# Kernel optimization log

Measured on AMD Instinct MI355X. Metric: run time of the kernel, lower is better.

The kernel has to match this reference:

```python
import jax, jax.numpy as jnp
import numpy as np

DIM = 768
HEADS = 12
HEAD_DIM = DIM // HEADS
SCALE = HEAD_DIM ** -0.5


def setup_inputs() -> dict:
    key = jax.random.key(0)
    k_x, k_qkv, k_ow, k_ob = jax.random.split(key, 4)
    B, N = 8, 1024
    x = jax.random.normal(k_x, (B, N, DIM), dtype=jnp.float32)
    # nn.Linear weights: out = x @ W.T + b; store torch-layout [out, in]
    w_qkv = jax.random.normal(k_qkv, (3 * DIM, DIM), dtype=jnp.float32) * (DIM ** -0.5)
    w_out = jax.random.normal(k_ow, (DIM, DIM), dtype=jnp.float32) * (DIM ** -0.5)
    b_out = jax.random.normal(k_ob, (DIM,), dtype=jnp.float32) * 0.01
    return {"x": x, "w_qkv": w_qkv, "w_out": w_out, "b_out": b_out}


def reference(x, w_qkv, w_out, b_out):
    B, N, C = x.shape
    qkv = jnp.einsum('bnc,dc->bnd', x, w_qkv)            # [B, N, 3C]
    qkv = qkv.reshape(B, N, 3, HEADS, HEAD_DIM)
    qkv = jnp.transpose(qkv, (2, 0, 3, 1, 4))            # [3, B, H, N, Dh]
    q, k, v = qkv[0], qkv[1], qkv[2]
    attn = jnp.einsum('bhqd,bhkd->bhqk', q, k) * SCALE   # [B, H, N, N]
    attn = jax.nn.softmax(attn, axis=-1)
    o = jnp.einsum('bhqk,bhkd->bhqd', attn, v)           # [B, H, N, Dh]
    o = jnp.transpose(o, (0, 2, 1, 3)).reshape(B, N, C)
    return jnp.einsum('bnc,dc->bnd', o, w_out) + b_out
```

## Files before the change

kernel.cpp:

```cpp
#include <hip/hip_runtime.h>

#define B_ 8
#define N_ 1024
#define DIM_ 768
#define H_ 12
#define DH_ 64
#define M_ (B_ * N_)
#define NQKV_ (3 * DIM_)
#define SCL_ 0.18033688011112042f

typedef unsigned short u16;
typedef unsigned int u32;
typedef __attribute__((ext_vector_type(8))) unsigned short u16x8;
typedef __attribute__((ext_vector_type(4))) unsigned short u16x4;
typedef __attribute__((ext_vector_type(8))) short bf16x8;
typedef __attribute__((ext_vector_type(4))) float f32x4;

__device__ __forceinline__ u16 f2bf(float f) {
  u32 u = __builtin_bit_cast(u32, f);
  u += 0x7fffu + ((u >> 16) & 1u);
  return (u16)(u >> 16);
}
__device__ __forceinline__ float bf2f(u16 v) {
  u32 u = ((u32)v) << 16;
  return __builtin_bit_cast(float, u);
}
__device__ __forceinline__ u32 cvtpk_bf16(float lo, float hi) {
  u32 r;
  asm("v_cvt_pk_bf16_f32 %0, %1, %2" : "=v"(r) : "v"(lo), "v"(hi));
  return r;
}
__device__ __forceinline__ void async16(const void* g, void* l) {
  __builtin_amdgcn_global_load_lds(
      (const __attribute__((address_space(1))) unsigned int*)g,
      (__attribute__((address_space(3))) unsigned int*)l, 16, 0, 0);
}

__global__ __launch_bounds__(256) void cast_bf16_k(const float* __restrict__ in,
                                                   u16* __restrict__ out, int n4) {
  int i = blockIdx.x * 256 + threadIdx.x;
  if (i >= n4) return;
  float4 v = reinterpret_cast<const float4*>(in)[i];
  u16x4 o;
  o.x = f2bf(v.x); o.y = f2bf(v.y); o.z = f2bf(v.z); o.w = f2bf(v.w);
  reinterpret_cast<u16x4*>(out)[i] = o;
}

template <bool OUT_BF16, bool BIAS, bool VSPLIT>
__global__ __launch_bounds__(256) void gemm_bt_k(
    const u16* __restrict__ A, const u16* __restrict__ Bm,
    void* __restrict__ Cv, const float* __restrict__ bias, int K, int ldc,
    u16* __restrict__ vT) {
  __shared__ u16 As[128 * 32];
  __shared__ u16 Bs[128 * 32];
  const int t = threadIdx.x;
  const int lane = t & 63;
  const int wid = t >> 6;
  const int brow = blockIdx.y << 7;
  const int bcol = blockIdx.x << 7;
  const int wrow = (wid >> 1) << 6;
  const int wcol = (wid & 1) << 6;

  f32x4 acc[4][4];
#pragma unroll
  for (int m = 0; m < 4; ++m)
#pragma unroll
    for (int n = 0; n < 4; ++n) acc[m][n] = (f32x4){0.f, 0.f, 0.f, 0.f};

  const int loff0 = t << 4, loff1 = (t + 256) << 4;
  const int r0 = loff0 >> 6, r1 = loff1 >> 6;
  const int s0 = ((((loff0 >> 4) & 3) ^ (r0 & 3)) << 3);
  const int s1 = ((((loff1 >> 4) & 3) ^ (r1 & 3)) << 3);
  const u16* gA0 = A + (size_t)(brow + r0) * K + s0;
  const u16* gA1 = A + (size_t)(brow + r1) * K + s1;
  const u16* gB0 = Bm + (size_t)(bcol + r0) * K + s0;
  const u16* gB1 = Bm + (size_t)(bcol + r1) * K + s1;
  char* lA = (char*)As;
  char* lB = (char*)Bs;

  const int kb = (lane >> 4) << 4;
  int aoff[4], boff[4];
#pragma unroll
  for (int m = 0; m < 4; ++m) {
    int ra = wrow + (m << 4) + (lane & 15);
    aoff[m] = (ra << 6) + (kb ^ ((ra & 3) << 4));
    int rb = wcol + (m << 4) + (lane & 15);
    boff[m] = (rb << 6) + (kb ^ ((rb & 3) << 4));
  }

  const int nkt = K >> 5;
  for (int kt = 0; kt < nkt; ++kt) {
    const int ko = kt << 5;
    async16(gA0 + ko, lA + loff0);
    async16(gA1 + ko, lA + loff1);
    async16(gB0 + ko, lB + loff0);
    async16(gB1 + ko, lB + loff1);
    __syncthreads();
    bf16x8 af[4], bfr[4];
#pragma unroll
    for (int m = 0; m < 4; ++m) af[m] = *(const bf16x8*)(lA + aoff[m]);
#pragma unroll
    for (int n = 0; n < 4; ++n) bfr[n] = *(const bf16x8*)(lB + boff[n]);
#pragma unroll
    for (int m = 0; m < 4; ++m)
#pragma unroll
      for (int n = 0; n < 4; ++n)
        acc[m][n] = __builtin_amdgcn_mfma_f32_16x16x32_bf16(af[m], bfr[n],
                                                            acc[m][n], 0, 0, 0);
    __syncthreads();
  }

  const int crow = brow + wrow + ((lane >> 4) << 2);
  const int ccol0 = bcol + wcol + (lane & 15);
  if (VSPLIT && bcol >= 2 * DIM_) {
#pragma unroll
    for (int n = 0; n < 4; ++n) {
      int colh = ccol0 + (n << 4) - 2 * DIM_;
      int h = colh >> 6, d = colh & 63;
#pragma unroll
      for (int m = 0; m < 4; ++m) {
        int row0 = crow + (m << 4);
        int bb = row0 >> 10, nn = row0 & 1023;
        int hbl = bb * H_ + h;
        uint2 pk;
        pk.x = (u32)f2bf(acc[m][n][0]) | ((u32)f2bf(acc[m][n][1]) << 16);
        pk.y = (u32)f2bf(acc[m][n][2]) | ((u32)f2bf(acc[m][n][3]) << 16);
        *(uint2*)(vT + (((size_t)(hbl * 64 + d)) << 10) + nn) = pk;
      }
    }
    return;
  }
#pragma unroll
  for (int m = 0; m < 4; ++m)
#pragma unroll
    for (int n = 0; n < 4; ++n) {
      int col = ccol0 + (n << 4);
      float bv = BIAS ? bias[col] : 0.f;
#pragma unroll
      for (int j = 0; j < 4; ++j) {
        int row = crow + (m << 4) + j;
        if (OUT_BF16)
          ((u16*)Cv)[(size_t)row * ldc + col] = f2bf(acc[m][n][j]);
        else
          ((float*)Cv)[(size_t)row * ldc + col] = acc[m][n][j] + bv;
      }
    }
}

__global__ __launch_bounds__(256) void attn_k(const u16* __restrict__ qkv,
                                              const u16* __restrict__ vT,
                                              u16* __restrict__ ob) {
  __shared__ u16 Ks[2][64 * 64];
  __shared__ u16 Vt[2][64 * 64];
  __shared__ u16 Ps[4][16 * 64];
  const int t = threadIdx.x;
  const int lane = t & 63;
  const int w = t >> 6;
  const int g = lane >> 4;
  const int q15 = lane & 15;

  const int orig = blockIdx.x;
  const int sub = orig >> 3;
  const int hb = (orig & 7) * 12 + (sub >> 4);
  const int qt = sub & 15;
  const int b = hb / H_;
  const int h = hb - b * H_;
  const int rowbase = b * N_;
  const int qcol = h * DH_;
  const int kcol = DIM_ + qcol;

  bf16x8 qf[2];
  {
    const int qrow = rowbase + (qt << 6) + (w << 4) + q15;
    const u16* src = qkv + (size_t)qrow * NQKV_ + qcol + (g << 3);
#pragma unroll
    for (int ks = 0; ks < 2; ++ks) {
      u16x8 raw = *(const u16x8*)(src + ks * 32);
      bf16x8 o;
#pragma unroll
      for (int j = 0; j < 8; ++j) o[j] = (short)f2bf(bf2f(raw[j]) * SCL_);
      qf[ks] = o;
    }
  }

  float mrow = -1e30f, lrow = 0.f;
  f32x4 oacc[4];
#pragma unroll
  for (int d = 0; d < 4; ++d) oacc[d] = (f32x4){0.f, 0.f, 0.f, 0.f};

  const int sr = t >> 3;
  const int c8 = t & 7;
  const int loff0 = t << 4, loff1 = (t + 256) << 4;
  const u16* kg0 = qkv + (size_t)(rowbase + sr) * NQKV_ + kcol + ((c8 ^ (sr & 7)) << 3);
  const u16* kg1 = qkv + (size_t)(rowbase + sr + 32) * NQKV_ + kcol + ((c8 ^ (sr & 7)) << 3);
  const u16* vg0 = vT + (((size_t)(hb * 64 + sr)) << 10) + ((c8 ^ (sr & 7)) << 3);
  const u16* vg1 = vT + (((size_t)(hb * 64 + sr + 32)) << 10) + ((c8 ^ (sr & 7)) << 3);
  char* lk0 = (char*)Ks;
  char* lv0 = (char*)Vt;
  char* lp = (char*)Ps + (w << 11);

  const int rowB = q15 << 7;
  const int xsw = (q15 & 7) << 4;
  const int x0 = (g << 4) ^ xsw;
  const int x1 = (64 + (g << 4)) ^ xsw;

  async16(kg0, lk0 + loff0);
  async16(kg1, lk0 + loff1);
  async16(vg0, lv0 + loff0);
  async16(vg1, lv0 + loff1);
  asm volatile("s_waitcnt vmcnt(0)" ::: "memory");
  __builtin_amdgcn_s_barrier();

  for (int kv = 0; kv < 16; ++kv) {
    const int cur = kv & 1;
    if (kv < 15) {
      const int nb = (cur ^ 1) << 13;
      const size_t kofs = (size_t)(kv + 1) * 64;
      async16(kg0 + kofs * NQKV_, lk0 + nb + loff0);
      async16(kg1 + kofs * NQKV_, lk0 + nb + loff1);
      async16(vg0 + kofs, lv0 + nb + loff0);
      async16(vg1 + kofs, lv0 + nb + loff1);
    }
    const char* lkc = lk0 + (cur << 13);
    const char* lvc = lv0 + (cur << 13);

    f32x4 s4[4];
#pragma unroll
    for (int n = 0; n < 4; ++n) s4[n] = (f32x4){0.f, 0.f, 0.f, 0.f};
    __builtin_amdgcn_s_setprio(1);
#pragma unroll
    for (int n = 0; n < 4; ++n) {
      bf16x8 kf0 = *(const bf16x8*)(lkc + (n << 11) + rowB + x0);
      s4[n] = __builtin_amdgcn_mfma_f32_16x16x32_bf16(kf0, qf[0], s4[n], 0, 0, 0);
      bf16x8 kf1 = *(const bf16x8*)(lkc + (n << 11) + rowB + x1);
      s4[n] = __builtin_amdgcn_mfma_f32_16x16x32_bf16(kf1, qf[1], s4[n], 0, 0, 0);
    }
    __builtin_amdgcn_s_setprio(0);

    float mx;
    {
      float a0 = fmaxf(fmaxf(s4[0][0], s4[0][1]), fmaxf(s4[0][2], s4[0][3]));
      float a1 = fmaxf(fmaxf(s4[1][0], s4[1][1]), fmaxf(s4[1][2], s4[1][3]));
      float a2 = fmaxf(fmaxf(s4[2][0], s4[2][1]), fmaxf(s4[2][2], s4[2][3]));
      float a3 = fmaxf(fmaxf(s4[3][0], s4[3][1]), fmaxf(s4[3][2], s4[3][3]));
      mx = fmaxf(fmaxf(a0, a1), fmaxf(a2, a3));
      mx = fmaxf(mx, __shfl_xor(mx, 16, 64));
      mx = fmaxf(mx, __shfl_xor(mx, 32, 64));
    }
    if (!__all(mx - mrow <= 8.f)) {
      float mn = fmaxf(mrow, mx);
      float al = __builtin_amdgcn_exp2f(mrow - mn);
      mrow = mn;
      lrow *= al;
      float alj[4];
#pragma unroll
      for (int j = 0; j < 4; ++j) alj[j] = __shfl(al, (g << 2) + j, 64);
#pragma unroll
      for (int d = 0; d < 4; ++d)
#pragma unroll
        for (int j = 0; j < 4; ++j) oacc[d][j] *= alj[j];
    }

    float p[4][4];
    float ps = 0.f;
#pragma unroll
    for (int n = 0; n < 4; ++n)
#pragma unroll
      for (int j = 0; j < 4; ++j) {
        p[n][j] = __builtin_amdgcn_exp2f(s4[n][j] - mrow);
        ps += p[n][j];
      }
    ps += __shfl_xor(ps, 16, 64);
    ps += __shfl_xor(ps, 32, 64);
    lrow += ps;

#pragma unroll
    for (int n = 0; n < 4; ++n) {
      uint2 pk;
      pk.x = cvtpk_bf16(p[n][0], p[n][1]);
      pk.y = cvtpk_bf16(p[n][2], p[n][3]);
      *(uint2*)(lp + rowB + (((n << 5) + (g << 3)) ^ xsw)) = pk;
    }

    bf16x8 pf0 = *(const bf16x8*)(lp + rowB + x0);
    bf16x8 pf1 = *(const bf16x8*)(lp + rowB + x1);
    __builtin_amdgcn_s_setprio(1);
#pragma unroll
    for (int dt = 0; dt < 4; ++dt) {
      bf16x8 vf0 = *(const bf16x8*)(lvc + (dt << 11) + rowB + x0);
      oacc[dt] = __builtin_amdgcn_mfma_f32_16x16x32_bf16(pf0, vf0, oacc[dt], 0, 0, 0);
      bf16x8 vf1 = *(const bf16x8*)(lvc + (dt << 11) + rowB + x1);
      oacc[dt] = __builtin_amdgcn_mfma_f32_16x16x32_bf16(pf1, vf1, oacc[dt], 0, 0, 0);
    }
    __builtin_amdgcn_s_setprio(0);

    asm volatile("s_waitcnt vmcnt(0)" ::: "memory");
    __builtin_amdgcn_s_barrier();
    __builtin_amdgcn_sched_barrier(0);
  }

  float rl = 1.f / lrow;
  float rlj[4];
#pragma unroll
  for (int j = 0; j < 4; ++j) rlj[j] = __shfl(rl, (g << 2) + j, 64);
  const int orow0 = rowbase + (qt << 6) + (w << 4) + (g << 2);
#pragma unroll
  for (int dt = 0; dt < 4; ++dt) {
    int col = qcol + (dt << 4) + q15;
#pragma unroll
    for (int j = 0; j < 4; ++j)
      ob[(size_t)(orow0 + j) * DIM_ + col] = f2bf(oacc[dt][j] * rlj[j]);
  }
}

extern "C" void kernel_launch(void* const* d_in, const int* in_sizes, int n_in,
                              void* d_out, int out_size, void* d_ws, size_t ws_size,
                              hipStream_t stream) {
  const float* x = (const float*)d_in[0];
  const float* w_qkv = (const float*)d_in[1];
  const float* w_out = (const float*)d_in[2];
  const float* b_out = (const float*)d_in[3];

  u16* xb = (u16*)d_ws;
  u16* wqkvb = xb + (size_t)M_ * DIM_;
  u16* woutb = wqkvb + (size_t)NQKV_ * DIM_;
  u16* qkvb = woutb + (size_t)DIM_ * DIM_;
  u16* obuf = qkvb + (size_t)M_ * NQKV_;
  u16* vT = obuf + (size_t)M_ * DIM_;

  {
    int n4 = M_ * DIM_ / 4;
    cast_bf16_k<<<(n4 + 255) / 256, 256, 0, stream>>>(x, xb, n4);
  }
  {
    int n4 = NQKV_ * DIM_ / 4;
    cast_bf16_k<<<(n4 + 255) / 256, 256, 0, stream>>>(w_qkv, wqkvb, n4);
  }
  {
    int n4 = DIM_ * DIM_ / 4;
    cast_bf16_k<<<(n4 + 255) / 256, 256, 0, stream>>>(w_out, woutb, n4);
  }

  gemm_bt_k<true, false, true><<<dim3(NQKV_ / 128, M_ / 128), 256, 0, stream>>>(
      xb, wqkvb, (void*)qkvb, nullptr, DIM_, NQKV_, vT);

  attn_k<<<dim3(B_ * H_ * 16), 256, 0, stream>>>(qkvb, vT, obuf);

  gemm_bt_k<false, true, false><<<dim3(DIM_ / 128, M_ / 128), 256, 0, stream>>>(
      obuf, woutb, d_out, b_out, DIM_, DIM_, nullptr);
}
```

Measured before the change: 213.2 us.

## Double-buffer GEMM LDS tiles and unroll attention loop by two

The QKV and output-projection GEMM kernel moves from a single LDS buffer, where each k-step loads and then waits, to a double-buffered ping-pong scheme. The next tile's async global-to-LDS load is issued before computing on the current one, with one vmcnt wait and barrier per step. The attention loop, which was already double-buffered, is unrolled by two with compile-time buffer offsets and incrementing pointers, removing runtime buffer selection. This doubles GEMM LDS use to 32KB per block, which could reduce occupancy.

```diff
diff --git a/kernel.cpp b/kernel.cpp
--- a/kernel.cpp
+++ b/kernel.cpp
@@ -35,6 +35,10 @@
       (const __attribute__((address_space(1))) unsigned int*)g,
       (__attribute__((address_space(3))) unsigned int*)l, 16, 0, 0);
 }
+#define VMCNT0_BARRIER()                                \
+  asm volatile("s_waitcnt vmcnt(0)" ::: "memory");      \
+  __builtin_amdgcn_s_barrier();                         \
+  __builtin_amdgcn_sched_barrier(0)
 
 __global__ __launch_bounds__(256) void cast_bf16_k(const float* __restrict__ in,
                                                    u16* __restrict__ out, int n4) {
@@ -46,13 +50,31 @@
   reinterpret_cast<u16x4*>(out)[i] = o;
 }
 
+template <int BUFO>
+__device__ __forceinline__ void gemm_step(const char* lA, const char* lB,
+                                          const int (&aoff)[4],
+                                          const int (&boff)[4],
+                                          f32x4 (&acc)[4][4]) {
+  bf16x8 af[4], bfr[4];
+#pragma unroll
+  for (int m = 0; m < 4; ++m) af[m] = *(const bf16x8*)(lA + BUFO + aoff[m]);
+#pragma unroll
+  for (int n = 0; n < 4; ++n) bfr[n] = *(const bf16x8*)(lB + BUFO + boff[n]);
+#pragma unroll
+  for (int m = 0; m < 4; ++m)
+#pragma unroll
+    for (int n = 0; n < 4; ++n)
+      acc[m][n] = __builtin_amdgcn_mfma_f32_16x16x32_bf16(af[m], bfr[n],
+                                                          acc[m][n], 0, 0, 0);
+}
+
 template <bool OUT_BF16, bool BIAS, bool VSPLIT>
 __global__ __launch_bounds__(256) void gemm_bt_k(
     const u16* __restrict__ A, const u16* __restrict__ Bm,
     void* __restrict__ Cv, const float* __restrict__ bias, int K, int ldc,
     u16* __restrict__ vT) {
-  __shared__ u16 As[128 * 32];
-  __shared__ u16 Bs[128 * 32];
+  __shared__ u16 As[2][128 * 32];
+  __shared__ u16 Bs[2][128 * 32];
   const int t = threadIdx.x;
   const int lane = t & 63;
   const int wid = t >> 6;
@@ -71,12 +93,21 @@
   const int r0 = loff0 >> 6, r1 = loff1 >> 6;
   const int s0 = ((((loff0 >> 4) & 3) ^ (r0 & 3)) << 3);
   const int s1 = ((((loff1 >> 4) & 3) ^ (r1 & 3)) << 3);
-  const u16* gA0 = A + (size_t)(brow + r0) * K + s0;
-  const u16* gA1 = A + (size_t)(brow + r1) * K + s1;
-  const u16* gB0 = Bm + (size_t)(bcol + r0) * K + s0;
-  const u16* gB1 = Bm + (size_t)(bcol + r1) * K + s1;
+  const u16* pA0 = A + (size_t)(brow + r0) * K + s0;
+  const u16* pA1 = A + (size_t)(brow + r1) * K + s1;
+  const u16* pB0 = Bm + (size_t)(bcol + r0) * K + s0;
+  const u16* pB1 = Bm + (size_t)(bcol + r1) * K + s1;
   char* lA = (char*)As;
   char* lB = (char*)Bs;
+
+#define GSTAGE(BUFO)                              \
+  do {                                            \
+    async16(pA0, lA + (BUFO) + loff0);            \
+    async16(pA1, lA + (BUFO) + loff1);            \
+    async16(pB0, lB + (BUFO) + loff0);            \
+    async16(pB1, lB + (BUFO) + loff1);            \
+    pA0 += 32; pA1 += 32; pB0 += 32; pB1 += 32;   \
+  } while (0)
 
   const int kb = (lane >> 4) << 4;
   int aoff[4], boff[4];
@@ -89,26 +120,17 @@
   }
 
   const int nkt = K >> 5;
-  for (int kt = 0; kt < nkt; ++kt) {
-    const int ko = kt << 5;
-    async16(gA0 + ko, lA + loff0);
-    async16(gA1 + ko, lA + loff1);
-    async16(gB0 + ko, lB + loff0);
-    async16(gB1 + ko, lB + loff1);
-    __syncthreads();
-    bf16x8 af[4], bfr[4];
-#pragma unroll
-    for (int m = 0; m < 4; ++m) af[m] = *(const bf16x8*)(lA + aoff[m]);
-#pragma unroll
-    for (int n = 0; n < 4; ++n) bfr[n] = *(const bf16x8*)(lB + boff[n]);
-#pragma unroll
-    for (int m = 0; m < 4; ++m)
-#pragma unroll
-      for (int n = 0; n < 4; ++n)
-        acc[m][n] = __builtin_amdgcn_mfma_f32_16x16x32_bf16(af[m], bfr[n],
-                                                            acc[m][n], 0, 0, 0);
-    __syncthreads();
-  }
+  GSTAGE(0);
+  VMCNT0_BARRIER();
+  for (int kt = 0; kt < nkt; kt += 2) {
+    GSTAGE(8192);
+    gemm_step<0>(lA, lB, aoff, boff, acc);
+    VMCNT0_BARRIER();
+    if (kt + 2 < nkt) GSTAGE(0);
+    gemm_step<8192>(lA, lB, aoff, boff, acc);
+    VMCNT0_BARRIER();
+  }
+#undef GSTAGE
 
   const int crow = brow + wrow + ((lane >> 4) << 2);
   const int ccol0 = bcol + wcol + (lane & 15);
@@ -147,6 +169,84 @@
     }
 }
 
+template <int KOFF, int VOFF>
+__device__ __forceinline__ void attn_tile(const char* lk0, const char* lv0,
+                                          char* lp, const bf16x8 (&qf)[2],
+                                          f32x4 (&oacc)[4], float& mrow,
+                                          float& lrow, const int rowB,
+                                          const int xsw, const int x0,
+                                          const int x1, const int g) {
+  f32x4 s4[4];
+#pragma unroll
+  for (int n = 0; n < 4; ++n) s4[n] = (f32x4){0.f, 0.f, 0.f, 0.f};
+  __builtin_amdgcn_s_setprio(1);
+#pragma unroll
+  for (int n = 0; n < 4; ++n) {
+    bf16x8 kf0 = *(const bf16x8*)(lk0 + KOFF + (n << 11) + rowB + x0);
+    s4[n] = __builtin_amdgcn_mfma_f32_16x16x32_bf16(kf0, qf[0], s4[n], 0, 0, 0);
+    bf16x8 kf1 = *(const bf16x8*)(lk0 + KOFF + (n << 11) + rowB + x1);
+    s4[n] = __builtin_amdgcn_mfma_f32_16x16x32_bf16(kf1, qf[1], s4[n], 0, 0, 0);
+  }
+  __builtin_amdgcn_s_setprio(0);
+
+  float mx;
+  {
+    float a0 = fmaxf(fmaxf(s4[0][0], s4[0][1]), fmaxf(s4[0][2], s4[0][3]));
+    float a1 = fmaxf(fmaxf(s4[1][0], s4[1][1]), fmaxf(s4[1][2], s4[1][3]));
+    float a2 = fmaxf(fmaxf(s4[2][0], s4[2][1]), fmaxf(s4[2][2], s4[2][3]));
+    float a3 = fmaxf(fmaxf(s4[3][0], s4[3][1]), fmaxf(s4[3][2], s4[3][3]));
+    mx = fmaxf(fmaxf(a0, a1), fmaxf(a2, a3));
+    mx = fmaxf(mx, __shfl_xor(mx, 16, 64));
+    mx = fmaxf(mx, __shfl_xor(mx, 32, 64));
+  }
+  if (!__all(mx - mrow <= 8.f)) {
+    float mn = fmaxf(mrow, mx);
+    float al = __builtin_amdgcn_exp2f(mrow - mn);
+    mrow = mn;
+    lrow *= al;
+    float alj[4];
+#pragma unroll
+    for (int j = 0; j < 4; ++j) alj[j] = __shfl(al, (g << 2) + j, 64);
+#pragma unroll
+    for (int d = 0; d < 4; ++d)
+#pragma unroll
+      for (int j = 0; j < 4; ++j) oacc[d][j] *= alj[j];
+  }
+
+  float p[4][4];
+  float ps = 0.f;
+#pragma unroll
+  for (int n = 0; n < 4; ++n)
+#pragma unroll
+    for (int j = 0; j < 4; ++j) {
+      p[n][j] = __builtin_amdgcn_exp2f(s4[n][j] - mrow);
+      ps += p[n][j];
+    }
+  ps += __shfl_xor(ps, 16, 64);
+  ps += __shfl_xor(ps, 32, 64);
+  lrow += ps;
+
+#pragma unroll
+  for (int n = 0; n < 4; ++n) {
+    uint2 pk;
+    pk.x = cvtpk_bf16(p[n][0], p[n][1]);
+    pk.y = cvtpk_bf16(p[n][2], p[n][3]);
+    *(uint2*)(lp + rowB + (((n << 5) + (g << 3)) ^ xsw)) = pk;
+  }
+
+  bf16x8 pf0 = *(const bf16x8*)(lp + rowB + x0);
+  bf16x8 pf1 = *(const bf16x8*)(lp + rowB + x1);
+  __builtin_amdgcn_s_setprio(1);
+#pragma unroll
+  for (int dt = 0; dt < 4; ++dt) {
+    bf16x8 vf0 = *(const bf16x8*)(lv0 + VOFF + (dt << 11) + rowB + x0);
+    oacc[dt] = __builtin_amdgcn_mfma_f32_16x16x32_bf16(pf0, vf0, oacc[dt], 0, 0, 0);
+    bf16x8 vf1 = *(const bf16x8*)(lv0 + VOFF + (dt << 11) + rowB + x1);
+    oacc[dt] = __builtin_amdgcn_mfma_f32_16x16x32_bf16(pf1, vf1, oacc[dt], 0, 0, 0);
+  }
+  __builtin_amdgcn_s_setprio(0);
+}
+
 __global__ __launch_bounds__(256) void attn_k(const u16* __restrict__ qkv,
                                               const u16* __restrict__ vT,
                                               u16* __restrict__ ob) {
@@ -191,113 +291,40 @@
   const int sr = t >> 3;
   const int c8 = t & 7;
   const int loff0 = t << 4, loff1 = (t + 256) << 4;
-  const u16* kg0 = qkv + (size_t)(rowbase + sr) * NQKV_ + kcol + ((c8 ^ (sr & 7)) << 3);
-  const u16* kg1 = qkv + (size_t)(rowbase + sr + 32) * NQKV_ + kcol + ((c8 ^ (sr & 7)) << 3);
-  const u16* vg0 = vT + (((size_t)(hb * 64 + sr)) << 10) + ((c8 ^ (sr & 7)) << 3);
-  const u16* vg1 = vT + (((size_t)(hb * 64 + sr + 32)) << 10) + ((c8 ^ (sr & 7)) << 3);
+  const u16* pk0 = qkv + (size_t)(rowbase + sr) * NQKV_ + kcol + ((c8 ^ (sr & 7)) << 3);
+  const u16* pk1 = qkv + (size_t)(rowbase + sr + 32) * NQKV_ + kcol + ((c8 ^ (sr & 7)) << 3);
+  const u16* pv0 = vT + (((size_t)(hb * 64 + sr)) << 10) + ((c8 ^ (sr & 7)) << 3);
+  const u16* pv1 = vT + (((size_t)(hb * 64 + sr + 32)) << 10) + ((c8 ^ (sr & 7)) << 3);
   char* lk0 = (char*)Ks;
   char* lv0 = (char*)Vt;
   char* lp = (char*)Ps + (w << 11);
+
+#define ASTAGE(BUFO)                                       \
+  do {                                                     \
+    async16(pk0, lk0 + (BUFO) + loff0);                    \
+    async16(pk1, lk0 + (BUFO) + loff1);                    \
+    async16(pv0, lv0 + (BUFO) + loff0);                    \
+    async16(pv1, lv0 + (BUFO) + loff1);                    \
+    pk0 += (size_t)64 * NQKV_; pk1 += (size_t)64 * NQKV_;  \
+    pv0 += 64; pv1 += 64;                                  \
+  } while (0)
 
   const int rowB = q15 << 7;
   const int xsw = (q15 & 7) << 4;
   const int x0 = (g << 4) ^ xsw;
   const int x1 = (64 + (g << 4)) ^ xsw;
 
-  async16(kg0, lk0 + loff0);
-  async16(kg1, lk0 + loff1);
-  async16(vg0, lv0 + loff0);
-  async16(vg1, lv0 + loff1);
-  asm volatile("s_waitcnt vmcnt(0)" ::: "memory");
-  __builtin_amdgcn_s_barrier();
-
-  for (int kv = 0; kv < 16; ++kv) {
-    const int cur = kv & 1;
-    if (kv < 15) {
-      const int nb = (cur ^ 1) << 13;
-      const size_t kofs = (size_t)(kv + 1) * 64;
-      async16(kg0 + kofs * NQKV_, lk0 + nb + loff0);
-      async16(kg1 + kofs * NQKV_, lk0 + nb + loff1);
-      async16(vg0 + kofs, lv0 + nb + loff0);
-      async16(vg1 + kofs, lv0 + nb + loff1);
-    }
-    const char* lkc = lk0 + (cur << 13);
-    const char* lvc = lv0 + (cur << 13);
-
-    f32x4 s4[4];
-#pragma unroll
-    for (int n = 0; n < 4; ++n) s4[n] = (f32x4){0.f, 0.f, 0.f, 0.f};
-    __builtin_amdgcn_s_setprio(1);
-#pragma unroll
-    for (int n = 0; n < 4; ++n) {
-      bf16x8 kf0 = *(const bf16x8*)(lkc + (n << 11) + rowB + x0);
-      s4[n] = __builtin_amdgcn_mfma_f32_16x16x32_bf16(kf0, qf[0], s4[n], 0, 0, 0);
-      bf16x8 kf1 = *(const bf16x8*)(lkc + (n << 11) + rowB + x1);
-      s4[n] = __builtin_amdgcn_mfma_f32_16x16x32_bf16(kf1, qf[1], s4[n], 0, 0, 0);
-    }
-    __builtin_amdgcn_s_setprio(0);
-
-    float mx;
-    {
-      float a0 = fmaxf(fmaxf(s4[0][0], s4[0][1]), fmaxf(s4[0][2], s4[0][3]));
-      float a1 = fmaxf(fmaxf(s4[1][0], s4[1][1]), fmaxf(s4[1][2], s4[1][3]));
-      float a2 = fmaxf(fmaxf(s4[2][0], s4[2][1]), fmaxf(s4[2][2], s4[2][3]));
-      float a3 = fmaxf(fmaxf(s4[3][0], s4[3][1]), fmaxf(s4[3][2], s4[3][3]));
-      mx = fmaxf(fmaxf(a0, a1), fmaxf(a2, a3));
-      mx = fmaxf(mx, __shfl_xor(mx, 16, 64));
-      mx = fmaxf(mx, __shfl_xor(mx, 32, 64));
-    }
-    if (!__all(mx - mrow <= 8.f)) {
-      float mn = fmaxf(mrow, mx);
-      float al = __builtin_amdgcn_exp2f(mrow - mn);
-      mrow = mn;
-      lrow *= al;
-      float alj[4];
-#pragma unroll
-      for (int j = 0; j < 4; ++j) alj[j] = __shfl(al, (g << 2) + j, 64);
-#pragma unroll
-      for (int d = 0; d < 4; ++d)
-#pragma unroll
-        for (int j = 0; j < 4; ++j) oacc[d][j] *= alj[j];
-    }
-
-    float p[4][4];
-    float ps = 0.f;
-#pragma unroll
-    for (int n = 0; n < 4; ++n)
-#pragma unroll
-      for (int j = 0; j < 4; ++j) {
-        p[n][j] = __builtin_amdgcn_exp2f(s4[n][j] - mrow);
-        ps += p[n][j];
-      }
-    ps += __shfl_xor(ps, 16, 64);
-    ps += __shfl_xor(ps, 32, 64);
-    lrow += ps;
-
-#pragma unroll
-    for (int n = 0; n < 4; ++n) {
-      uint2 pk;
-      pk.x = cvtpk_bf16(p[n][0], p[n][1]);
-      pk.y = cvtpk_bf16(p[n][2], p[n][3]);
-      *(uint2*)(lp + rowB + (((n << 5) + (g << 3)) ^ xsw)) = pk;
-    }
-
-    bf16x8 pf0 = *(const bf16x8*)(lp + rowB + x0);
-    bf16x8 pf1 = *(const bf16x8*)(lp + rowB + x1);
-    __builtin_amdgcn_s_setprio(1);
-#pragma unroll
-    for (int dt = 0; dt < 4; ++dt) {
-      bf16x8 vf0 = *(const bf16x8*)(lvc + (dt << 11) + rowB + x0);
-      oacc[dt] = __builtin_amdgcn_mfma_f32_16x16x32_bf16(pf0, vf0, oacc[dt], 0, 0, 0);
-      bf16x8 vf1 = *(const bf16x8*)(lvc + (dt << 11) + rowB + x1);
-      oacc[dt] = __builtin_amdgcn_mfma_f32_16x16x32_bf16(pf1, vf1, oacc[dt], 0, 0, 0);
-    }
-    __builtin_amdgcn_s_setprio(0);
-
-    asm volatile("s_waitcnt vmcnt(0)" ::: "memory");
-    __builtin_amdgcn_s_barrier();
-    __builtin_amdgcn_sched_barrier(0);
-  }
+  ASTAGE(0);
+  VMCNT0_BARRIER();
+  for (int kvt = 0; kvt < 16; kvt += 2) {
+    ASTAGE(8192);
+    attn_tile<0, 0>(lk0, lv0, lp, qf, oacc, mrow, lrow, rowB, xsw, x0, x1, g);
+    VMCNT0_BARRIER();
+    if (kvt < 14) ASTAGE(0);
+    attn_tile<8192, 8192>(lk0, lv0, lp, qf, oacc, mrow, lrow, rowB, xsw, x0, x1, g);
+    VMCNT0_BARRIER();
+  }
+#undef ASTAGE
 
   float rl = 1.f / lrow;
   float rlj[4];
```

Result: no change. 211.6 us (-0.8%).
